# Optimization experiments

Measured on AMD Instinct MI355X. Metric: run time of the kernel, lower is better.

## Reference

```python
import jax, jax.numpy as jnp
import numpy as np


def setup_inputs() -> dict:
    key = jax.random.key(0)
    ks = jax.random.split(key, 7)
    B, N, D = 32, 512, 64
    H = D // 2
    return {
        "receiver": jax.random.normal(ks[0], (B, N, D), dtype=jnp.float32),
        "attendant": jax.random.normal(ks[1], (B, N, D), dtype=jnp.float32),
        "adj_mask": jax.random.uniform(ks[2], (B, N, N), dtype=jnp.float32),
        "w_q": jax.random.normal(ks[3], (D, H), dtype=jnp.float32) * (1.0 / np.sqrt(D)),
        "w_k": jax.random.normal(ks[4], (D, H), dtype=jnp.float32) * (1.0 / np.sqrt(D)),
        "bias": jax.random.normal(ks[5], (H,), dtype=jnp.float32) * 0.1,
        "a": jax.random.normal(ks[6], (H,), dtype=jnp.float32) * 0.1,
    }


def reference(receiver, attendant, adj_mask, w_q, w_k, bias, a):
    # keys: [B,N,H], queries: [B,N,H]
    keys = receiver @ w_k
    queries = attendant @ w_q
    # additive (GAT-style) scores: broadcast-add -> tanh -> dot with a
    # e_act: [B, N, M, H]  (N from keys, M from queries, matching torch unsqueeze(-3)/(-2))
    e_act = jnp.tanh(queries[:, None, :, :] + keys[:, :, None, :] + bias)
    e_scores = jnp.einsum("bnmh,h->bnm", e_act, a)
    # masked projection: adj @ scores @ adj
    att = jnp.einsum("bnk,bkm->bnm", adj_mask, e_scores)
    att = jnp.einsum("bnk,bkm->bnm", att, adj_mask)
    return att
```

## Files before the change

### kernel.cpp

```cpp
#include <hip/hip_runtime.h>

#define GN 512
#define HH 32
#define DD 64

typedef float v4f __attribute__((ext_vector_type(4)));
typedef unsigned int v4u __attribute__((ext_vector_type(4)));
typedef u_int32_t u32;
typedef u32 v2u __attribute__((ext_vector_type(2)));
typedef __bf16 v8bf __attribute__((ext_vector_type(8)));

__device__ __forceinline__ u32 f2bf(float f) {
  u32 u = __builtin_bit_cast(u32, f);
  return (u + 0x7fffu + ((u >> 16) & 1u)) >> 16;
}
__device__ __forceinline__ u32 pack2(float a, float b) {
  return f2bf(a) | (f2bf(b) << 16);
}

#define GLOAD16(g, l)                                                              \
  __builtin_amdgcn_global_load_lds((const __attribute__((address_space(1))) u32*)(g), \
                                   (__attribute__((address_space(3))) u32*)(l), 16, 0, 0)
#define VMCNT0 asm volatile("s_waitcnt vmcnt(0)" ::: "memory")
#define SCHEDBAR __builtin_amdgcn_sched_barrier(0)

__global__ __launch_bounds__(256) void kq_kernel(const float* __restrict__ rec,
                                                 const float* __restrict__ att,
                                                 const float* __restrict__ wq,
                                                 const float* __restrict__ wk,
                                                 const float* __restrict__ bias,
                                                 float* __restrict__ ekbuf,
                                                 float* __restrict__ eqbuf) {
  __shared__ float rr[512], ra[512];
  int tid = threadIdx.x;
  size_t base = (size_t)blockIdx.x * 8;
  const float* gr = rec + base * DD;
  const float* ga = att + base * DD;
  rr[tid] = gr[tid]; rr[tid + 256] = gr[tid + 256];
  ra[tid] = ga[tid]; ra[tid + 256] = ga[tid + 256];
  __syncthreads();
  int r = tid >> 5, h = tid & 31;
  float sk = bias[h], sq = 0.f;
  const float* rrow = &rr[r * DD];
  const float* arow = &ra[r * DD];
#pragma unroll 8
  for (int d = 0; d < DD; ++d) {
    sk += rrow[d] * wk[d * HH + h];
    sq += arow[d] * wq[d * HH + h];
  }
  const float C = 2.8853900817779268f;
  ekbuf[(base + r) * HH + h] = __builtin_exp2f(C * sk);
  eqbuf[(base + r) * HH + h] = __builtin_exp2f(C * sq);
}

__global__ __launch_bounds__(256) void prep_kernel(const float* __restrict__ adj,
                                                   const float* __restrict__ ek,
                                                   const float* __restrict__ eq,
                                                   const float* __restrict__ avec,
                                                   unsigned short* __restrict__ adjT,
                                                   unsigned short* __restrict__ adjBF,
                                                   unsigned short* __restrict__ Et) {
  __shared__ __align__(16) float tA[64 * 64];
  __shared__ __align__(16) float kl[64 * 32];
  __shared__ __align__(16) float ql[64 * 32];

  int tid = threadIdx.x, wave = tid >> 6;
  int b = blockIdx.z;
  int n0 = blockIdx.x * 64, m0 = blockIdx.y * 64;
  int c0 = n0, r0 = m0;

  v4f a2v[8];
  float asum = 0.f;
#pragma unroll
  for (int h4 = 0; h4 < 8; ++h4) {
    v4f av = *(const v4f*)(avec + h4 * 4);
    a2v[h4] = av * 2.0f;
    asum += av[0] + av[1] + av[2] + av[3];
  }
  SCHEDBAR;

  const float* kb = ek + ((size_t)b * GN + n0) * HH;
  const float* qb = eq + ((size_t)b * GN + m0) * HH;
#pragma unroll
  for (int i = 0; i < 2; ++i) {
    int c = i * 256 + tid;
    int r = c >> 3, g = (c & 7) ^ (r & 7);
    GLOAD16(kb + r * HH + g * 4, (char*)kl + (i * 256 + wave * 64) * 16);
    GLOAD16(qb + r * HH + g * 4, (char*)ql + (i * 256 + wave * 64) * 16);
  }
  SCHEDBAR;
  const float* ab = adj + (size_t)b * GN * GN;
#pragma unroll
  for (int i = 0; i < 4; ++i) {
    int c = i * 256 + tid;
    int r = c >> 4, g = (c & 15) ^ (r & 15);
    GLOAD16(ab + (size_t)(r0 + r) * GN + c0 + g * 4, (char*)tA + (i * 256 + wave * 64) * 16);
  }
  SCHEDBAR;
  asm volatile("s_waitcnt vmcnt(4)" ::: "memory");
  __builtin_amdgcn_s_barrier();
  SCHEDBAR;

  int m = tid >> 2, ng = tid & 3;
  v4f qv[8];
#pragma unroll
  for (int h4 = 0; h4 < 8; ++h4)
    qv[h4] = *(const v4f*)&ql[m * HH + ((h4 ^ (m & 7)) << 2)];
  int x0 = 2 * ng, x1 = 2 * ng + 1;
  u32 ow[8];
#pragma unroll
  for (int nn = 0; nn < 8; ++nn) {
    int n = ng * 2 + nn * 8;
    v4f acc0 = (v4f){0.f, 0.f, 0.f, 0.f};
    v4f acc1 = (v4f){0.f, 0.f, 0.f, 0.f};
#pragma unroll
    for (int h4 = 0; h4 < 8; ++h4) {
      v4f kv0 = *(const v4f*)&kl[n * HH + ((h4 ^ x0) << 2)];
      v4f kv1 = *(const v4f*)&kl[(n + 1) * HH + ((h4 ^ x1) << 2)];
      v4f f0 = kv0 * qv[h4] + 1.0f;
      v4f f1 = kv1 * qv[h4] + 1.0f;
      v4f r0v, r1v;
#pragma unroll
      for (int e = 0; e < 4; ++e) {
        r0v[e] = __builtin_amdgcn_rcpf(f0[e]);
        r1v[e] = __builtin_amdgcn_rcpf(f1[e]);
      }
      acc0 += a2v[h4] * r0v;
      acc1 += a2v[h4] * r1v;
    }
    float s0 = asum - (acc0[0] + acc0[1] + acc0[2] + acc0[3]);
    float s1 = asum - (acc1[0] + acc1[1] + acc1[2] + acc1[3]);
    ow[nn] = pack2(s0, s1);
  }

  VMCNT0;
  __builtin_amdgcn_s_barrier();
  SCHEDBAR;

  unsigned short* of = adjBF + (size_t)b * GN * GN;
#pragma unroll
  for (int i = 0; i < 4; ++i) {
    int c = i * 256 + tid;
    int r = c >> 4, g = (c & 15) ^ (r & 15);
    v4f f = *(const v4f*)&tA[c * 4];
    v2u pk = {pack2(f[0], f[1]), pack2(f[2], f[3])};
    *(v2u*)(of + (size_t)(r0 + r) * GN + c0 + g * 4) = pk;
  }
  {
    unsigned short* ob = adjT + (size_t)b * GN * GN;
    int col = tid & 63, rs = (tid >> 6) * 16;
    int gc = col >> 2, ce = col & 3;
    u32 qq[8];
#pragma unroll
    for (int j = 0; j < 8; ++j) {
      int R0 = rs + 2 * j, R1 = R0 + 1;
      float v0 = tA[R0 * 64 + ((gc ^ (R0 & 15)) << 2) + ce];
      float v1 = tA[R1 * 64 + ((gc ^ (R1 & 15)) << 2) + ce];
      qq[j] = pack2(v0, v1);
    }
    unsigned short* dst = ob + (size_t)(c0 + col) * GN + r0 + rs;
    *(v4u*)dst = (v4u){qq[0], qq[1], qq[2], qq[3]};
    *(v4u*)(dst + 8) = (v4u){qq[4], qq[5], qq[6], qq[7]};
  }
  u32* dstw = (u32*)(Et + ((size_t)b * GN + m0 + m) * GN + n0);
#pragma unroll
  for (int nn = 0; nn < 8; ++nn) dstw[ng + nn * 4] = ow[nn];
}

#define SWZ(r, s) ((s) ^ ((r) & 7))

template <bool OUTF32>
__global__ __launch_bounds__(256) void gemm_bt(const unsigned short* __restrict__ A,
                                               const unsigned short* __restrict__ Bt,
                                               void* __restrict__ Cv) {
  __shared__ unsigned short At[2][128 * 64];
  __shared__ unsigned short Bs[2][128 * 64];
  int bid = blockIdx.x;
  int swz = (bid & 7) * 64 + (bid >> 3);
  int b = swz >> 4;
  int row0 = ((swz >> 2) & 3) * 128;
  int col0 = (swz & 3) * 128;
  int tid = threadIdx.x, lane = tid & 63, wave = tid >> 6;
  int wr = wave >> 1, wc = wave & 1;
  const unsigned short* Ab = A + (size_t)b * GN * GN;
  const unsigned short* Bb = Bt + (size_t)b * GN * GN;

  v4f acc[4][4];
#pragma unroll
  for (int i = 0; i < 4; ++i)
#pragma unroll
    for (int j = 0; j < 4; ++j) acc[i][j] = (v4f){0.f, 0.f, 0.f, 0.f};

  int cc_r[4], cc_s[4];
#pragma unroll
  for (int i = 0; i < 4; ++i) {
    int c = i * 256 + tid;
    cc_r[i] = c >> 3;
    cc_s[i] = SWZ(c >> 3, c & 7);
  }

#define STAGE(buf, kt)                                                                   \
  {                                                                                      \
    _Pragma("unroll") for (int i = 0; i < 4; ++i) {                                      \
      const unsigned short* ga = Ab + (size_t)(row0 + cc_r[i]) * GN + (kt)*64 + cc_s[i] * 8; \
      const unsigned short* gb = Bb + (size_t)(col0 + cc_r[i]) * GN + (kt)*64 + cc_s[i] * 8; \
      GLOAD16(ga, (char*)&At[buf][0] + (i * 256 + wave * 64) * 16);                      \
      GLOAD16(gb, (char*)&Bs[buf][0] + (i * 256 + wave * 64) * 16);                      \
    }                                                                                    \
  }

#define COMPUTE(buf)                                                                     \
  {                                                                                      \
    int lr = lane & 15, s16 = lane >> 4;                                                 \
    _Pragma("unroll") for (int h = 0; h < 2; ++h) {                                      \
      int sl = h * 4 + s16;                                                              \
      v8bf af[4], bfv[4];                                                                \
      _Pragma("unroll") for (int i = 0; i < 4; ++i) {                                    \
        int r = wr * 64 + i * 16 + lr;                                                   \
        af[i] = *(const v8bf*)&At[buf][r * 64 + SWZ(r, sl) * 8];                         \
      }                                                                                  \
      _Pragma("unroll") for (int j = 0; j < 4; ++j) {                                    \
        int r = wc * 64 + j * 16 + lr;                                                   \
        bfv[j] = *(const v8bf*)&Bs[buf][r * 64 + SWZ(r, sl) * 8];                        \
      }                                                                                  \
      _Pragma("unroll") for (int i = 0; i < 4; ++i)                                      \
          _Pragma("unroll") for (int j = 0; j < 4; ++j) acc[i][j] =                      \
          __builtin_amdgcn_mfma_f32_16x16x32_bf16(af[i], bfv[j], acc[i][j], 0, 0, 0);    \
    }                                                                                    \
  }

  STAGE(0, 0);
  VMCNT0;
  __builtin_amdgcn_s_barrier();
#pragma unroll
  for (int kt = 0; kt < 7; ++kt) {
    int cur = kt & 1;
    STAGE(cur ^ 1, kt + 1);
    COMPUTE(cur);
    VMCNT0;
    __builtin_amdgcn_s_barrier();
  }
  COMPUTE(1);

  int lc = lane & 15;
  int lrow4 = (lane >> 4) * 4;
#pragma unroll
  for (int i = 0; i < 4; ++i) {
#pragma unroll
    for (int j = 0; j < 4; ++j) {
      int gr = row0 + wr * 64 + i * 16 + lrow4;
      int gc = col0 + wc * 64 + j * 16 + lc;
#pragma unroll
      for (int e = 0; e < 4; ++e) {
        float v = acc[i][j][e];
        if constexpr (OUTF32)
          ((float*)Cv)[(size_t)b * GN * GN + (size_t)(gr + e) * GN + gc] = v;
        else
          ((unsigned short*)Cv)[(size_t)b * GN * GN + (size_t)(gr + e) * GN + gc] =
              (unsigned short)f2bf(v);
      }
    }
  }
#undef STAGE
#undef COMPUTE
}

extern "C" void kernel_launch(void* const* d_in, const int* in_sizes, int n_in,
                              void* d_out, int out_size, void* d_ws, size_t ws_size,
                              hipStream_t stream) {
  const float* receiver  = (const float*)d_in[0];
  const float* attendant = (const float*)d_in[1];
  const float* adj       = (const float*)d_in[2];
  const float* wq        = (const float*)d_in[3];
  const float* wk        = (const float*)d_in[4];
  const float* bias      = (const float*)d_in[5];
  const float* avec      = (const float*)d_in[6];
  float* out = (float*)d_out;

  char* ws = (char*)d_ws;
  float* ekbuf          = (float*)(ws);
  float* eqbuf          = (float*)(ws + (2u << 20));
  unsigned short* Et    = (unsigned short*)(ws + (4u << 20));
  unsigned short* adjT  = (unsigned short*)(ws + (20u << 20));
  unsigned short* adjBF = (unsigned short*)(ws + (36u << 20));
  unsigned short* Tbuf  = (unsigned short*)(ws + (52u << 20));

  kq_kernel<<<dim3(2048), dim3(256), 0, stream>>>(receiver, attendant, wq, wk, bias,
                                                  ekbuf, eqbuf);
  prep_kernel<<<dim3(8, 8, 32), dim3(256), 0, stream>>>(adj, ekbuf, eqbuf, avec,
                                                        adjT, adjBF, Et);
  gemm_bt<false><<<dim3(512), dim3(256), 0, stream>>>(adjBF, Et, Tbuf);
  gemm_bt<true><<<dim3(512), dim3(256), 0, stream>>>(Tbuf, adjT, out);
}
```

Before: 80.78 us.

## Register-tile the tanh score computation 4x4 per thread with padded LDS rows

```diff
diff --git a/kernel.cpp b/kernel.cpp
--- a/kernel.cpp
+++ b/kernel.cpp
@@ -61,33 +61,21 @@
                                                    unsigned short* __restrict__ adjBF,
                                                    unsigned short* __restrict__ Et) {
   __shared__ __align__(16) float tA[64 * 64];
-  __shared__ __align__(16) float kl[64 * 32];
-  __shared__ __align__(16) float ql[64 * 32];
+  __shared__ __align__(16) float kl[64 * 36];
+  __shared__ __align__(16) float ql[64 * 36];
 
   int tid = threadIdx.x, wave = tid >> 6;
   int b = blockIdx.z;
   int n0 = blockIdx.x * 64, m0 = blockIdx.y * 64;
   int c0 = n0, r0 = m0;
 
-  v4f a2v[8];
-  float asum = 0.f;
-#pragma unroll
-  for (int h4 = 0; h4 < 8; ++h4) {
-    v4f av = *(const v4f*)(avec + h4 * 4);
-    a2v[h4] = av * 2.0f;
-    asum += av[0] + av[1] + av[2] + av[3];
-  }
-  SCHEDBAR;
-
   const float* kb = ek + ((size_t)b * GN + n0) * HH;
   const float* qb = eq + ((size_t)b * GN + m0) * HH;
-#pragma unroll
-  for (int i = 0; i < 2; ++i) {
-    int c = i * 256 + tid;
-    int r = c >> 3, g = (c & 7) ^ (r & 7);
-    GLOAD16(kb + r * HH + g * 4, (char*)kl + (i * 256 + wave * 64) * 16);
-    GLOAD16(qb + r * HH + g * 4, (char*)ql + (i * 256 + wave * 64) * 16);
-  }
+  int sr = tid >> 3, sp = tid & 7;
+  v4f rk0 = *(const v4f*)(kb + sr * HH + sp * 4);
+  v4f rq0 = *(const v4f*)(qb + sr * HH + sp * 4);
+  v4f rk1 = *(const v4f*)(kb + (sr + 32) * HH + sp * 4);
+  v4f rq1 = *(const v4f*)(qb + (sr + 32) * HH + sp * 4);
   SCHEDBAR;
   const float* ab = adj + (size_t)b * GN * GN;
 #pragma unroll
@@ -97,41 +85,63 @@
     GLOAD16(ab + (size_t)(r0 + r) * GN + c0 + g * 4, (char*)tA + (i * 256 + wave * 64) * 16);
   }
   SCHEDBAR;
+
+  float a2s[HH];
+  float asum = 0.f;
+#pragma unroll
+  for (int h = 0; h < HH; ++h) {
+    float av = avec[h];
+    a2s[h] = 2.0f * av;
+    asum += av;
+  }
+
   asm volatile("s_waitcnt vmcnt(4)" ::: "memory");
+  *(v4f*)&kl[sr * 36 + sp * 4] = rk0;
+  *(v4f*)&ql[sr * 36 + sp * 4] = rq0;
+  *(v4f*)&kl[(sr + 32) * 36 + sp * 4] = rk1;
+  *(v4f*)&ql[(sr + 32) * 36 + sp * 4] = rq1;
+  asm volatile("s_waitcnt lgkmcnt(0)" ::: "memory");
   __builtin_amdgcn_s_barrier();
   SCHEDBAR;
 
-  int m = tid >> 2, ng = tid & 3;
-  v4f qv[8];
-#pragma unroll
-  for (int h4 = 0; h4 < 8; ++h4)
-    qv[h4] = *(const v4f*)&ql[m * HH + ((h4 ^ (m & 7)) << 2)];
-  int x0 = 2 * ng, x1 = 2 * ng + 1;
-  u32 ow[8];
-#pragma unroll
-  for (int nn = 0; nn < 8; ++nn) {
-    int n = ng * 2 + nn * 8;
-    v4f acc0 = (v4f){0.f, 0.f, 0.f, 0.f};
-    v4f acc1 = (v4f){0.f, 0.f, 0.f, 0.f};
-#pragma unroll
-    for (int h4 = 0; h4 < 8; ++h4) {
-      v4f kv0 = *(const v4f*)&kl[n * HH + ((h4 ^ x0) << 2)];
-      v4f kv1 = *(const v4f*)&kl[(n + 1) * HH + ((h4 ^ x1) << 2)];
-      v4f f0 = kv0 * qv[h4] + 1.0f;
-      v4f f1 = kv1 * qv[h4] + 1.0f;
-      v4f r0v, r1v;
-#pragma unroll
-      for (int e = 0; e < 4; ++e) {
-        r0v[e] = __builtin_amdgcn_rcpf(f0[e]);
-        r1v[e] = __builtin_amdgcn_rcpf(f1[e]);
+  int mg = tid >> 4, ng = tid & 15;
+  const float* kvb[4];
+  const float* qvb[4];
+#pragma unroll
+  for (int j = 0; j < 4; ++j) {
+    kvb[j] = &kl[(ng + 16 * j) * 36];
+    qvb[j] = &ql[(mg + 16 * j) * 36];
+  }
+  float acc[4][4];
+#pragma unroll
+  for (int i = 0; i < 4; ++i)
+#pragma unroll
+    for (int j = 0; j < 4; ++j) acc[i][j] = 0.f;
+
+#pragma unroll
+  for (int h4 = 0; h4 < 8; ++h4) {
+    v4f kv[4], qv[4];
+#pragma unroll
+    for (int j = 0; j < 4; ++j) kv[j] = *(const v4f*)(kvb[j] + h4 * 4);
+#pragma unroll
+    for (int i = 0; i < 4; ++i) qv[i] = *(const v4f*)(qvb[i] + h4 * 4);
+#pragma unroll
+    for (int i = 0; i < 4; ++i)
+#pragma unroll
+      for (int j = 0; j < 4; ++j) {
+        v4f f = kv[j] * qv[i] + 1.0f;
+        acc[i][j] = __builtin_fmaf(a2s[h4 * 4 + 0], __builtin_amdgcn_rcpf(f[0]), acc[i][j]);
+        acc[i][j] = __builtin_fmaf(a2s[h4 * 4 + 1], __builtin_amdgcn_rcpf(f[1]), acc[i][j]);
+        acc[i][j] = __builtin_fmaf(a2s[h4 * 4 + 2], __builtin_amdgcn_rcpf(f[2]), acc[i][j]);
+        acc[i][j] = __builtin_fmaf(a2s[h4 * 4 + 3], __builtin_amdgcn_rcpf(f[3]), acc[i][j]);
       }
-      acc0 += a2v[h4] * r0v;
-      acc1 += a2v[h4] * r1v;
-    }
-    float s0 = asum - (acc0[0] + acc0[1] + acc0[2] + acc0[3]);
-    float s1 = asum - (acc1[0] + acc1[1] + acc1[2] + acc1[3]);
-    ow[nn] = pack2(s0, s1);
-  }
+  }
+  unsigned short* eb = Et + ((size_t)b * GN + m0 + mg) * GN + n0 + ng;
+#pragma unroll
+  for (int i = 0; i < 4; ++i)
+#pragma unroll
+    for (int j = 0; j < 4; ++j)
+      eb[(size_t)(16 * i) * GN + 16 * j] = (unsigned short)f2bf(asum - acc[i][j]);
 
   VMCNT0;
   __builtin_amdgcn_s_barrier();
@@ -162,9 +172,6 @@
     *(v4u*)dst = (v4u){qq[0], qq[1], qq[2], qq[3]};
     *(v4u*)(dst + 8) = (v4u){qq[4], qq[5], qq[6], qq[7]};
   }
-  u32* dstw = (u32*)(Et + ((size_t)b * GN + m0 + m) * GN + n0);
-#pragma unroll
-  for (int nn = 0; nn < 8; ++nn) dstw[ng + nn * 4] = ow[nn];
 }
 
 #define SWZ(r, s) ((s) ^ ((r) & 7))
```

Measured after the change: 79.76 us. Within noise of the previous version (-1.3%).
